# Performance work log

Hardware: AMD Instinct MI355X
Metric: run time of the kernel (lower is better)

## Reference

```python
import jax, jax.numpy as jnp
import numpy as np

LATENT_SIZE = 1024
WORD_SIZE = 64
NB_WORD = 8192
COMMIT_VQ = 2.5
BATCH = 2048


def setup_inputs() -> dict:
    key = jax.random.key(0)
    k1, k2, k3 = jax.random.split(key, 3)
    z_mean = jax.random.normal(k1, (BATCH, LATENT_SIZE), dtype=jnp.float32)
    z_log_var = jax.random.normal(k2, (BATCH, LATENT_SIZE), dtype=jnp.float32)
    # Embedding initialized uniform(-1/nb_word, 1/nb_word) in the torch module;
    # use normal here for a numerically non-degenerate correctness baseline.
    emb_weight = jax.random.normal(k3, (NB_WORD, WORD_SIZE), dtype=jnp.float32)
    return {"z_mean": z_mean, "z_log_var": z_log_var, "emb_weight": emb_weight}


def reference(z_mean, z_log_var, emb_weight):
    sg = jax.lax.stop_gradient
    input_shape = z_mean.shape
    # (B * latent/word, word)
    z = z_mean.reshape(-1, LATENT_SIZE // WORD_SIZE, WORD_SIZE)
    z_flat = z.reshape(-1, WORD_SIZE)
    # squared euclidean distances: (N, nb_word)
    distances = (
        jnp.sum(z_flat ** 2, axis=1, keepdims=True)
        + jnp.sum(emb_weight ** 2, axis=1)
        - 2.0 * jnp.einsum("bd,nd->bn", z_flat, emb_weight)
    )
    min_idx = jnp.argmin(distances, axis=1)  # (N,)
    z_q = emb_weight[min_idx].reshape(z.shape)  # gather codebook vectors
    loss = (
        jnp.mean((sg(z_q) - z) ** 2)
        + COMMIT_VQ * jnp.mean((z_q - sg(z)) ** 2)
    )
    z_q_st = z + sg(z_q - z)  # straight-through estimator
    return z_q_st.reshape(input_shape), loss
```

## Files before the change

kernel.cpp:

```cpp
#include <hip/hip_runtime.h>
#include <math.h>

#define LATENT   1024
#define WORD     64
#define NB_WORD  8192
#define BATCH    2048
#define NROWS    (BATCH * LATENT / WORD)
#define NELEM    (BATCH * LATENT)

#define NCHUNK   8
#define CWCHUNK  (NB_WORD / NCHUNK)
#define TPC      (CWCHUNK / 16)
#define NTILE    (NB_WORD / 16)
#define PKTS     (NTILE * 6 * 64)

typedef __attribute__((ext_vector_type(8))) __bf16 bf16x8;
typedef __attribute__((ext_vector_type(4))) float  f32x4;

__global__ __launch_bounds__(256) void vq_prep_kernel(
    const float* __restrict__ emb, float* __restrict__ e2,
    bf16x8* __restrict__ epack) {
    int m = blockIdx.x * 256 + threadIdx.x;
    int tile = m >> 4, l15 = m & 15;
    float s0 = 0.f, s1 = 0.f, s2 = 0.f, s3 = 0.f;
#pragma unroll
    for (int Ks = 0; Ks < 2; ++Ks) {
#pragma unroll
        for (int q = 0; q < 4; ++q) {
            const float4* s4 = reinterpret_cast<const float4*>(
                emb + (size_t)m * WORD + Ks * 32 + q * 8);
            float4 a = s4[0], b = s4[1];
            float tv[8] = {a.x, a.y, a.z, a.w, b.x, b.y, b.z, b.w};
            bf16x8 oh, om, ol;
#pragma unroll
            for (int e = 0; e < 8; ++e) {
                float v = tv[e];
                if ((e & 3) == 0) s0 = fmaf(v, v, s0);
                else if ((e & 3) == 1) s1 = fmaf(v, v, s1);
                else if ((e & 3) == 2) s2 = fmaf(v, v, s2);
                else s3 = fmaf(v, v, s3);
                __bf16 h  = (__bf16)v;
                float r1  = v - (float)h;
                __bf16 mm = (__bf16)r1;
                float r2  = r1 - (float)mm;
                __bf16 lo = (__bf16)r2;
                oh[e] = h; om[e] = mm; ol[e] = lo;
            }
            size_t base = ((size_t)tile * 6) * 64 + q * 16 + l15;
            epack[base + (size_t)(0 * 2 + Ks) * 64] = oh;
            epack[base + (size_t)(1 * 2 + Ks) * 64] = om;
            epack[base + (size_t)(2 * 2 + Ks) * 64] = ol;
        }
    }
    e2[m] = (s0 + s1) + (s2 + s3);
}

__device__ __forceinline__ void gload_lds16(const char* g, char* l) {
    __builtin_amdgcn_global_load_lds(
        (const __attribute__((address_space(1))) void*)g,
        (__attribute__((address_space(3))) void*)l, 16, 0, 0);
}

#define MFMA16 __builtin_amdgcn_mfma_f32_16x16x32_bf16

__global__ __launch_bounds__(256)
__attribute__((amdgpu_waves_per_eu(4, 4)))
void vq_argmin_kernel(
    const float* __restrict__ z, const bf16x8* __restrict__ epack,
    const float* __restrict__ e2, unsigned long long* __restrict__ best) {

    __shared__ __align__(16) char le[4][2][6144];

    const int tid   = threadIdx.x;
    const int lane  = tid & 63;
    const int wband = tid >> 6;
    const int l15   = lane & 15;
    const int l4    = lane >> 4;
    const int rowbase   = blockIdx.x * 128 + wband * 32;
    const int tile0     = blockIdx.y * TPC;
    const int chunkbase = blockIdx.y * CWCHUNK;
    const float* e2g    = e2 + chunkbase;
    const int off       = (blockIdx.x & 15) * 4;

    bf16x8 A[2][2][3];
    const float4* zf4 = reinterpret_cast<const float4*>(z);
#pragma unroll
    for (int mt = 0; mt < 2; ++mt) {
        int row = rowbase + mt * 16 + l15;
#pragma unroll
        for (int Ks = 0; Ks < 2; ++Ks) {
            float4 v0 = zf4[(size_t)row * 16 + Ks * 8 + l4 * 2];
            float4 v1 = zf4[(size_t)row * 16 + Ks * 8 + l4 * 2 + 1];
            float tv[8] = {v0.x, v0.y, v0.z, v0.w, v1.x, v1.y, v1.z, v1.w};
#pragma unroll
            for (int e = 0; e < 8; ++e) {
                float v = tv[e];
                __bf16 h  = (__bf16)v;
                float r1  = v - (float)h;
                __bf16 m  = (__bf16)r1;
                float r2  = r1 - (float)m;
                __bf16 lo = (__bf16)r2;
                A[mt][Ks][0][e] = h;
                A[mt][Ks][1][e] = m;
                A[mt][Ks][2][e] = lo;
            }
        }
    }

    char* lbase = &le[wband][0][0];

    {
        const char* src = (const char*)epack + (size_t)(tile0 + off) * 6144 + lane * 16;
#pragma unroll
        for (int j = 0; j < 6; ++j)
            gload_lds16(src + j * 1024, lbase + j * 1024);
    }
    float e2A = e2g[off * 16 + l15];
    float e2B;

    float bestd[8] = {INFINITY, INFINITY, INFINITY, INFINITY,
                      INFINITY, INFINITY, INFINITY, INFINITY};
    int   bt[8]    = {0, 0, 0, 0, 0, 0, 0, 0};

#define PHASE(BUFOFF, E2CUR, E2NXT, TCUR, TNXT)                             \
    {                                                                       \
        const char* srcn = (const char*)epack +                             \
                           (size_t)(tile0 + (TNXT)) * 6144 + lane * 16;     \
        char* dstn = lbase + ((BUFOFF) ^ 6144);                             \
        _Pragma("unroll")                                                   \
        for (int j = 0; j < 6; ++j)                                         \
            gload_lds16(srcn + j * 1024, dstn + j * 1024);                  \
        E2NXT = e2g[(TNXT) * 16 + l15];                                     \
        asm volatile("s_waitcnt vmcnt(7)" ::: "memory");                    \
        asm volatile("" :: "v"(E2CUR));         \
        const char* bb = lbase + (BUFOFF) + lane * 16;                      \
        bf16x8 Bh0 = *reinterpret_cast<const bf16x8*>(bb);                  \
        bf16x8 Bh1 = *reinterpret_cast<const bf16x8*>(bb + 1024);           \
        bf16x8 Bm0 = *reinterpret_cast<const bf16x8*>(bb + 2048);           \
        bf16x8 Bm1 = *reinterpret_cast<const bf16x8*>(bb + 3072);           \
        bf16x8 Bl0 = *reinterpret_cast<const bf16x8*>(bb + 4096);           \
        bf16x8 Bl1 = *reinterpret_cast<const bf16x8*>(bb + 5120);           \
        f32x4 a00 = {0.f, 0.f, 0.f, 0.f};                                   \
        f32x4 a01 = {0.f, 0.f, 0.f, 0.f};                                   \
        f32x4 a10 = {0.f, 0.f, 0.f, 0.f};                                   \
        f32x4 a11 = {0.f, 0.f, 0.f, 0.f};                                   \
          \
        a00 = MFMA16(A[0][0][0], Bh0, a00, 0, 0, 0);                        \
        a10 = MFMA16(A[1][0][0], Bh0, a10, 0, 0, 0);                        \
        a01 = MFMA16(A[0][1][0], Bh1, a01, 0, 0, 0);                        \
        a11 = MFMA16(A[1][1][0], Bh1, a11, 0, 0, 0);                        \
        a00 = MFMA16(A[0][0][1], Bh0, a00, 0, 0, 0);                        \
        a10 = MFMA16(A[1][0][1], Bh0, a10, 0, 0, 0);                        \
        a01 = MFMA16(A[0][1][1], Bh1, a01, 0, 0, 0);                        \
        a11 = MFMA16(A[1][1][1], Bh1, a11, 0, 0, 0);                        \
        a00 = MFMA16(A[0][0][2], Bh0, a00, 0, 0, 0);                        \
        a10 = MFMA16(A[1][0][2], Bh0, a10, 0, 0, 0);                        \
        a01 = MFMA16(A[0][1][2], Bh1, a01, 0, 0, 0);                        \
        a11 = MFMA16(A[1][1][2], Bh1, a11, 0, 0, 0);                        \
        a00 = MFMA16(A[0][0][1], Bm0, a00, 0, 0, 0);                        \
        a10 = MFMA16(A[1][0][1], Bm0, a10, 0, 0, 0);                        \
        a01 = MFMA16(A[0][1][1], Bm1, a01, 0, 0, 0);                        \
        a11 = MFMA16(A[1][1][1], Bm1, a11, 0, 0, 0);                        \
        a00 = MFMA16(A[0][0][0], Bm0, a00, 0, 0, 0);                        \
        a10 = MFMA16(A[1][0][0], Bm0, a10, 0, 0, 0);                        \
        a01 = MFMA16(A[0][1][0], Bm1, a01, 0, 0, 0);                        \
        a11 = MFMA16(A[1][1][0], Bm1, a11, 0, 0, 0);                        \
        a00 = MFMA16(A[0][0][0], Bl0, a00, 0, 0, 0);                        \
        a10 = MFMA16(A[1][0][0], Bl0, a10, 0, 0, 0);                        \
        a01 = MFMA16(A[0][1][0], Bl1, a01, 0, 0, 0);                        \
        a11 = MFMA16(A[1][1][0], Bl1, a11, 0, 0, 0);                        \
        _Pragma("unroll")                                                   \
        for (int v = 0; v < 4; ++v) {                                       \
            float d0 = fmaf(-2.0f, a00[v] + a01[v], E2CUR);                 \
            if (d0 < bestd[v])     { bestd[v]     = d0; bt[v]     = (TCUR); } \
            float d1 = fmaf(-2.0f, a10[v] + a11[v], E2CUR);                 \
            if (d1 < bestd[4 + v]) { bestd[4 + v] = d1; bt[4 + v] = (TCUR); } \
        }                                                                   \
    }

    int t0 = off;
    for (int tt = 0; tt < TPC; tt += 2) {
        int t1 = t0 + 1; if (t1 >= TPC) t1 -= TPC;
        int t2 = t1 + 1; if (t2 >= TPC) t2 -= TPC;
        PHASE(0,    e2A, e2B, t0, t1);
        PHASE(6144, e2B, e2A, t1, t2);
        t0 = t2;
    }
#undef PHASE

#pragma unroll
    for (int mt = 0; mt < 2; ++mt) {
#pragma unroll
        for (int v = 0; v < 4; ++v) {
            float bd = bestd[mt * 4 + v];
            int   cw = chunkbase + bt[mt * 4 + v] * 16 + l15;
            unsigned db = __float_as_uint(bd);
            db = (db & 0x80000000u) ? ~db : (db | 0x80000000u);
            unsigned long long key =
                ((unsigned long long)db << 32) | (unsigned)cw;
#pragma unroll
            for (int off2 = 1; off2 < 16; off2 <<= 1) {
                unsigned long long o = __shfl_xor(key, off2);
                key = (o < key) ? o : key;
            }
            if (l15 == 0)
                atomicMin(&best[rowbase + mt * 16 + l4 * 4 + v], key);
        }
    }
}

__global__ __launch_bounds__(256) void vq_out_kernel(
    const float* __restrict__ z, const float* __restrict__ emb,
    const unsigned long long* __restrict__ best,
    float* __restrict__ out, float* __restrict__ lsum) {
    const int base = (blockIdx.x * 256 + threadIdx.x) * 8;
    const int row  = base >> 6;
    const int m    = (int)(best[row] & 0xFFFFFFFFull);

    const float4* zp = reinterpret_cast<const float4*>(z + base);
    const float4* qp = reinterpret_cast<const float4*>(emb + (size_t)m * WORD + (base & 63));
    float4* op = reinterpret_cast<float4*>(out + base);

    float s = 0.f;
#pragma unroll
    for (int i = 0; i < 2; ++i) {
        float4 zv = zp[i];
        float4 qv = qp[i];
        float dx = qv.x - zv.x, dy = qv.y - zv.y, dz = qv.z - zv.z, dw = qv.w - zv.w;
        float4 ov;
        ov.x = zv.x + dx; ov.y = zv.y + dy; ov.z = zv.z + dz; ov.w = zv.w + dw;
        op[i] = ov;
        s += dx*dx + dy*dy + dz*dz + dw*dw;
    }

#pragma unroll
    for (int off = 32; off > 0; off >>= 1) s += __shfl_down(s, off);
    __shared__ float wsum[4];
    int lane = threadIdx.x & 63, wid = threadIdx.x >> 6;
    if (lane == 0) wsum[wid] = s;
    __syncthreads();
    if (threadIdx.x == 0)
        atomicAdd(lsum, (wsum[0] + wsum[1]) + (wsum[2] + wsum[3]));
}

__global__ void vq_loss_kernel(const float* __restrict__ lsum,
                               float* __restrict__ loss_out) {
    float mean = lsum[0] * (1.0f / (float)NELEM);
    loss_out[0] = mean + 2.5f * mean;
}

extern "C" void kernel_launch(void* const* d_in, const int* in_sizes, int n_in,
                              void* d_out, int out_size, void* d_ws, size_t ws_size,
                              hipStream_t stream) {
    const float* z   = (const float*)d_in[0];
    const float* emb = (const float*)d_in[2];
    float* out = (float*)d_out;

    bf16x8* epack = (bf16x8*)d_ws;
    float*  e2    = (float*)((char*)d_ws + (size_t)PKTS * 16);
    unsigned long long* best =
        (unsigned long long*)((char*)e2 + NB_WORD * sizeof(float));
    float* lsum = (float*)((char*)best + NROWS * sizeof(unsigned long long));

    hipMemsetAsync(best, 0xFF, NROWS * sizeof(unsigned long long), stream);
    hipMemsetAsync(lsum, 0, sizeof(float), stream);

    vq_prep_kernel<<<NB_WORD / 256, 256, 0, stream>>>(emb, e2, epack);
    vq_argmin_kernel<<<dim3(NROWS / 128, NCHUNK), 256, 0, stream>>>(
        z, epack, e2, best);
    vq_out_kernel<<<NELEM / (256 * 8), 256, 0, stream>>>(z, emb, best, out, lsum);
    vq_loss_kernel<<<1, 1, 0, stream>>>(lsum, out + NELEM);
}
```

Baseline: 222.3 us.

## Share codebook LDS tiles across waves and overlap argmin fold with MFMAs

The four waves of a block now cooperatively load one shared double-buffered codebook tile into LDS and synchronise with a block barrier, instead of each wave streaming its own private copy. The argmin fold for the previous tile is software-pipelined and interleaved between MFMA groups of the current tile using sched_barrier and setprio. Occupancy is pinned to 3 waves per EU, and blocks get staggered start delays via s_sleep. This cuts redundant global-to-LDS traffic and hides the fold latency, at the cost of a per-tile block barrier and lower occupancy.

```diff
diff --git a/kernel.cpp b/kernel.cpp
--- a/kernel.cpp
+++ b/kernel.cpp
@@ -62,14 +62,22 @@
 }
 
 #define MFMA16 __builtin_amdgcn_mfma_f32_16x16x32_bf16
+#define SBAR() __builtin_amdgcn_sched_barrier(0)
 
 __global__ __launch_bounds__(256)
-__attribute__((amdgpu_waves_per_eu(4, 4)))
+__attribute__((amdgpu_waves_per_eu(3, 3)))
 void vq_argmin_kernel(
     const float* __restrict__ z, const bf16x8* __restrict__ epack,
     const float* __restrict__ e2, unsigned long long* __restrict__ best) {
 
-    __shared__ __align__(16) char le[4][2][6144];
+    {
+        int ph = blockIdx.x & 3;
+        if (ph == 1) __builtin_amdgcn_s_sleep(2);
+        else if (ph == 2) __builtin_amdgcn_s_sleep(4);
+        else if (ph == 3) __builtin_amdgcn_s_sleep(6);
+    }
+
+    __shared__ __align__(16) char le[2 * 6144];
 
     const int tid   = threadIdx.x;
     const int lane  = tid & 63;
@@ -107,86 +115,101 @@
         }
     }
 
-    char* lbase = &le[wband][0][0];
-
     {
-        const char* src = (const char*)epack + (size_t)(tile0 + off) * 6144 + lane * 16;
-#pragma unroll
-        for (int j = 0; j < 6; ++j)
-            gload_lds16(src + j * 1024, lbase + j * 1024);
-    }
-    float e2A = e2g[off * 16 + l15];
-    float e2B;
+        const char* src = (const char*)epack + (size_t)(tile0 + off) * 6144;
+        gload_lds16(src + wband * 1024 + lane * 16, le + wband * 1024);
+        if (wband < 2)
+            gload_lds16(src + (4 + wband) * 1024 + lane * 16,
+                        le + (4 + wband) * 1024);
+    }
 
     float bestd[8] = {INFINITY, INFINITY, INFINITY, INFINITY,
                       INFINITY, INFINITY, INFINITY, INFINITY};
     int   bt[8]    = {0, 0, 0, 0, 0, 0, 0, 0};
 
-#define PHASE(BUFOFF, E2CUR, E2NXT, TCUR, TNXT)                             \
+    f32x4 x00, x01, x10, x11;
+    f32x4 y00 = {0.f,0.f,0.f,0.f}, y01 = {0.f,0.f,0.f,0.f};
+    f32x4 y10 = {0.f,0.f,0.f,0.f}, y11 = {0.f,0.f,0.f,0.f};
+    float e2x, e2y = INFINITY;
+
+#define FOLD1(P00,P01,P10,P11, E2P, TP, V)                                  \
+    do {                                                                    \
+        float d0_ = fmaf(-2.0f, P00[V] + P01[V], E2P);                      \
+        if (d0_ < bestd[V])     { bestd[V]     = d0_; bt[V]     = (TP); }   \
+        float d1_ = fmaf(-2.0f, P10[V] + P11[V], E2P);                      \
+        if (d1_ < bestd[4+(V)]) { bestd[4+(V)] = d1_; bt[4+(V)] = (TP); }   \
+    } while (0)
+
+#define GROUP(SPL, B0, B1, C00,C01,C10,C11)                                 \
+    C00 = MFMA16(A[0][0][SPL], B0, C00, 0, 0, 0);                           \
+    C10 = MFMA16(A[1][0][SPL], B0, C10, 0, 0, 0);                           \
+    C01 = MFMA16(A[0][1][SPL], B1, C01, 0, 0, 0);                           \
+    C11 = MFMA16(A[1][1][SPL], B1, C11, 0, 0, 0);
+
+#define PHASE(BUFOFF, C00,C01,C10,C11, P00,P01,P10,P11, E2C, E2P, TCUR, TNXT, TP) \
     {                                                                       \
-        const char* srcn = (const char*)epack +                             \
-                           (size_t)(tile0 + (TNXT)) * 6144 + lane * 16;     \
-        char* dstn = lbase + ((BUFOFF) ^ 6144);                             \
-        _Pragma("unroll")                                                   \
-        for (int j = 0; j < 6; ++j)                                         \
-            gload_lds16(srcn + j * 1024, dstn + j * 1024);                  \
-        E2NXT = e2g[(TNXT) * 16 + l15];                                     \
-        asm volatile("s_waitcnt vmcnt(7)" ::: "memory");                    \
-        asm volatile("" :: "v"(E2CUR));         \
-        const char* bb = lbase + (BUFOFF) + lane * 16;                      \
+        asm volatile("s_waitcnt vmcnt(0)" ::: "memory");                    \
+        SBAR();                                                             \
+        __builtin_amdgcn_s_barrier();          \
+        const char* bb = le + (BUFOFF) + lane * 16;                         \
         bf16x8 Bh0 = *reinterpret_cast<const bf16x8*>(bb);                  \
         bf16x8 Bh1 = *reinterpret_cast<const bf16x8*>(bb + 1024);           \
         bf16x8 Bm0 = *reinterpret_cast<const bf16x8*>(bb + 2048);           \
         bf16x8 Bm1 = *reinterpret_cast<const bf16x8*>(bb + 3072);           \
         bf16x8 Bl0 = *reinterpret_cast<const bf16x8*>(bb + 4096);           \
         bf16x8 Bl1 = *reinterpret_cast<const bf16x8*>(bb + 5120);           \
-        f32x4 a00 = {0.f, 0.f, 0.f, 0.f};                                   \
-        f32x4 a01 = {0.f, 0.f, 0.f, 0.f};                                   \
-        f32x4 a10 = {0.f, 0.f, 0.f, 0.f};                                   \
-        f32x4 a11 = {0.f, 0.f, 0.f, 0.f};                                   \
-          \
-        a00 = MFMA16(A[0][0][0], Bh0, a00, 0, 0, 0);                        \
-        a10 = MFMA16(A[1][0][0], Bh0, a10, 0, 0, 0);                        \
-        a01 = MFMA16(A[0][1][0], Bh1, a01, 0, 0, 0);                        \
-        a11 = MFMA16(A[1][1][0], Bh1, a11, 0, 0, 0);                        \
-        a00 = MFMA16(A[0][0][1], Bh0, a00, 0, 0, 0);                        \
-        a10 = MFMA16(A[1][0][1], Bh0, a10, 0, 0, 0);                        \
-        a01 = MFMA16(A[0][1][1], Bh1, a01, 0, 0, 0);                        \
-        a11 = MFMA16(A[1][1][1], Bh1, a11, 0, 0, 0);                        \
-        a00 = MFMA16(A[0][0][2], Bh0, a00, 0, 0, 0);                        \
-        a10 = MFMA16(A[1][0][2], Bh0, a10, 0, 0, 0);                        \
-        a01 = MFMA16(A[0][1][2], Bh1, a01, 0, 0, 0);                        \
-        a11 = MFMA16(A[1][1][2], Bh1, a11, 0, 0, 0);                        \
-        a00 = MFMA16(A[0][0][1], Bm0, a00, 0, 0, 0);                        \
-        a10 = MFMA16(A[1][0][1], Bm0, a10, 0, 0, 0);                        \
-        a01 = MFMA16(A[0][1][1], Bm1, a01, 0, 0, 0);                        \
-        a11 = MFMA16(A[1][1][1], Bm1, a11, 0, 0, 0);                        \
-        a00 = MFMA16(A[0][0][0], Bm0, a00, 0, 0, 0);                        \
-        a10 = MFMA16(A[1][0][0], Bm0, a10, 0, 0, 0);                        \
-        a01 = MFMA16(A[0][1][0], Bm1, a01, 0, 0, 0);                        \
-        a11 = MFMA16(A[1][1][0], Bm1, a11, 0, 0, 0);                        \
-        a00 = MFMA16(A[0][0][0], Bl0, a00, 0, 0, 0);                        \
-        a10 = MFMA16(A[1][0][0], Bl0, a10, 0, 0, 0);                        \
-        a01 = MFMA16(A[0][1][0], Bl1, a01, 0, 0, 0);                        \
-        a11 = MFMA16(A[1][1][0], Bl1, a11, 0, 0, 0);                        \
-        _Pragma("unroll")                                                   \
-        for (int v = 0; v < 4; ++v) {                                       \
-            float d0 = fmaf(-2.0f, a00[v] + a01[v], E2CUR);                 \
-            if (d0 < bestd[v])     { bestd[v]     = d0; bt[v]     = (TCUR); } \
-            float d1 = fmaf(-2.0f, a10[v] + a11[v], E2CUR);                 \
-            if (d1 < bestd[4 + v]) { bestd[4 + v] = d1; bt[4 + v] = (TCUR); } \
-        }                                                                   \
+        const char* srcn = (const char*)epack +                             \
+                           (size_t)(tile0 + (TNXT)) * 6144;                 \
+        char* dstn = le + ((BUFOFF) ^ 6144);                                \
+        gload_lds16(srcn + wband * 1024 + lane * 16, dstn + wband * 1024);  \
+        if (wband < 2)                                                      \
+            gload_lds16(srcn + (4 + wband) * 1024 + lane * 16,              \
+                        dstn + (4 + wband) * 1024);                         \
+        E2C = e2g[(TCUR) * 16 + l15];                                       \
+        __builtin_amdgcn_s_setprio(1);                                      \
+        SBAR();                                                             \
+                \
+        FOLD1(P00,P01,P10,P11, E2P, TP, 0);                                 \
+        FOLD1(P00,P01,P10,P11, E2P, TP, 1);                                 \
+        C00 = (f32x4){0.f,0.f,0.f,0.f};                                     \
+        C01 = (f32x4){0.f,0.f,0.f,0.f};                                     \
+        C10 = (f32x4){0.f,0.f,0.f,0.f};                                     \
+        C11 = (f32x4){0.f,0.f,0.f,0.f};                                     \
+        SBAR();                                                             \
+        GROUP(0, Bh0, Bh1, C00,C01,C10,C11)                         \
+        SBAR();                                                             \
+        FOLD1(P00,P01,P10,P11, E2P, TP, 2);                                 \
+        SBAR();                                                             \
+        GROUP(1, Bh0, Bh1, C00,C01,C10,C11)                         \
+        SBAR();                                                             \
+        FOLD1(P00,P01,P10,P11, E2P, TP, 3);                                 \
+        SBAR();                                                             \
+        GROUP(2, Bh0, Bh1, C00,C01,C10,C11)                         \
+        GROUP(1, Bm0, Bm1, C00,C01,C10,C11)                         \
+        GROUP(0, Bm0, Bm1, C00,C01,C10,C11)                         \
+        GROUP(0, Bl0, Bl1, C00,C01,C10,C11)                         \
+        __builtin_amdgcn_s_setprio(0);                                      \
     }
 
     int t0 = off;
+    int tp = 0;
     for (int tt = 0; tt < TPC; tt += 2) {
         int t1 = t0 + 1; if (t1 >= TPC) t1 -= TPC;
         int t2 = t1 + 1; if (t2 >= TPC) t2 -= TPC;
-        PHASE(0,    e2A, e2B, t0, t1);
-        PHASE(6144, e2B, e2A, t1, t2);
+        PHASE(0,    x00,x01,x10,x11, y00,y01,y10,y11, e2x, e2y, t0, t1, tp);
+        PHASE(6144, y00,y01,y10,y11, x00,x01,x10,x11, e2y, e2x, t1, t2, t0);
+        tp = t1;
         t0 = t2;
     }
 #undef PHASE
+
+    asm volatile("s_waitcnt vmcnt(0)" ::: "memory");
+    FOLD1(y00,y01,y10,y11, e2y, tp, 0);
+    FOLD1(y00,y01,y10,y11, e2y, tp, 1);
+    FOLD1(y00,y01,y10,y11, e2y, tp, 2);
+    FOLD1(y00,y01,y10,y11, e2y, tp, 3);
+#undef FOLD1
+#undef GROUP
 
 #pragma unroll
     for (int mt = 0; mt < 2; ++mt) {
```

New measurement: 200.1 us. 1.11x faster.

## Switch argmin to 32x32x16 MFMA with block-shared codebook tiles

Applied to the files above, without the earlier changes.

Replaces the 16x16x32 bf16 MFMA tiling with 32x32x16 tiles that cover 32 rows by 32 codewords per wave, so one accumulator holds the whole K=64 reduction. The codebook pack layout is changed to match, and the four waves now share one double-buffered LDS tile loaded cooperatively under a block barrier, instead of each wave keeping private buffers. It also staggers block start with s_sleep, raises MFMA priority with setprio, and lowers the occupancy target to 3 waves per EU. The aim is fewer B-operand loads and a better MFMA-to-overhead ratio, at the cost of a full vmcnt(0) wait plus barrier on every phase and wider 32-lane shuffle reductions.

```diff
diff --git a/kernel.cpp b/kernel.cpp
--- a/kernel.cpp
+++ b/kernel.cpp
@@ -10,47 +10,43 @@
 
 #define NCHUNK   8
 #define CWCHUNK  (NB_WORD / NCHUNK)
-#define TPC      (CWCHUNK / 16)
-#define NTILE    (NB_WORD / 16)
-#define PKTS     (NTILE * 6 * 64)
-
-typedef __attribute__((ext_vector_type(8))) __bf16 bf16x8;
-typedef __attribute__((ext_vector_type(4))) float  f32x4;
+#define TPC      32
+#define PKTS     (NB_WORD / 32 * 768)
+
+typedef __attribute__((ext_vector_type(8)))  __bf16 bf16x8;
+typedef __attribute__((ext_vector_type(16))) float  f32x16;
 
 __global__ __launch_bounds__(256) void vq_prep_kernel(
     const float* __restrict__ emb, float* __restrict__ e2,
     bf16x8* __restrict__ epack) {
     int m = blockIdx.x * 256 + threadIdx.x;
-    int tile = m >> 4, l15 = m & 15;
+    int tile = m >> 5, col = m & 31;
     float s0 = 0.f, s1 = 0.f, s2 = 0.f, s3 = 0.f;
 #pragma unroll
-    for (int Ks = 0; Ks < 2; ++Ks) {
-#pragma unroll
-        for (int q = 0; q < 4; ++q) {
-            const float4* s4 = reinterpret_cast<const float4*>(
-                emb + (size_t)m * WORD + Ks * 32 + q * 8);
-            float4 a = s4[0], b = s4[1];
-            float tv[8] = {a.x, a.y, a.z, a.w, b.x, b.y, b.z, b.w};
-            bf16x8 oh, om, ol;
-#pragma unroll
-            for (int e = 0; e < 8; ++e) {
-                float v = tv[e];
-                if ((e & 3) == 0) s0 = fmaf(v, v, s0);
-                else if ((e & 3) == 1) s1 = fmaf(v, v, s1);
-                else if ((e & 3) == 2) s2 = fmaf(v, v, s2);
-                else s3 = fmaf(v, v, s3);
-                __bf16 h  = (__bf16)v;
-                float r1  = v - (float)h;
-                __bf16 mm = (__bf16)r1;
-                float r2  = r1 - (float)mm;
-                __bf16 lo = (__bf16)r2;
-                oh[e] = h; om[e] = mm; ol[e] = lo;
-            }
-            size_t base = ((size_t)tile * 6) * 64 + q * 16 + l15;
-            epack[base + (size_t)(0 * 2 + Ks) * 64] = oh;
-            epack[base + (size_t)(1 * 2 + Ks) * 64] = om;
-            epack[base + (size_t)(2 * 2 + Ks) * 64] = ol;
+    for (int g = 0; g < 8; ++g) {
+        const float4* s4 = reinterpret_cast<const float4*>(
+            emb + (size_t)m * WORD + g * 8);
+        float4 a = s4[0], b = s4[1];
+        float tv[8] = {a.x, a.y, a.z, a.w, b.x, b.y, b.z, b.w};
+        bf16x8 oh, om, ol;
+#pragma unroll
+        for (int e = 0; e < 8; ++e) {
+            float v = tv[e];
+            if ((e & 3) == 0) s0 = fmaf(v, v, s0);
+            else if ((e & 3) == 1) s1 = fmaf(v, v, s1);
+            else if ((e & 3) == 2) s2 = fmaf(v, v, s2);
+            else s3 = fmaf(v, v, s3);
+            __bf16 h  = (__bf16)v;
+            float r1  = v - (float)h;
+            __bf16 mm = (__bf16)r1;
+            float r2  = r1 - (float)mm;
+            oh[e] = h; om[e] = mm; ol[e] = (__bf16)r2;
         }
+        int ks = g >> 1, hi = g & 1;
+        size_t pb = (size_t)tile * 768;
+        epack[pb + (size_t)(0 * 4 + ks) * 64 + hi * 32 + col] = oh;
+        epack[pb + (size_t)(1 * 4 + ks) * 64 + hi * 32 + col] = om;
+        epack[pb + (size_t)(2 * 4 + ks) * 64 + hi * 32 + col] = ol;
     }
     e2[m] = (s0 + s1) + (s2 + s3);
 }
@@ -61,36 +57,42 @@
         (__attribute__((address_space(3))) void*)l, 16, 0, 0);
 }
 
-#define MFMA16 __builtin_amdgcn_mfma_f32_16x16x32_bf16
+#define MFMA32 __builtin_amdgcn_mfma_f32_32x32x16_bf16
 
 __global__ __launch_bounds__(256)
-__attribute__((amdgpu_waves_per_eu(4, 4)))
+__attribute__((amdgpu_waves_per_eu(3, 3)))
 void vq_argmin_kernel(
     const float* __restrict__ z, const bf16x8* __restrict__ epack,
     const float* __restrict__ e2, unsigned long long* __restrict__ best) {
 
-    __shared__ __align__(16) char le[4][2][6144];
+    {
+        int ph = blockIdx.x & 3;
+        if (ph == 1) __builtin_amdgcn_s_sleep(2);
+        else if (ph == 2) __builtin_amdgcn_s_sleep(4);
+        else if (ph == 3) __builtin_amdgcn_s_sleep(6);
+    }
+
+    __shared__ __align__(16) char le[2 * 12288];
 
     const int tid   = threadIdx.x;
     const int lane  = tid & 63;
     const int wband = tid >> 6;
-    const int l15   = lane & 15;
-    const int l4    = lane >> 4;
+    const int l31   = lane & 31;
+    const int hi    = lane >> 5;
     const int rowbase   = blockIdx.x * 128 + wband * 32;
     const int tile0     = blockIdx.y * TPC;
     const int chunkbase = blockIdx.y * CWCHUNK;
     const float* e2g    = e2 + chunkbase;
-    const int off       = (blockIdx.x & 15) * 4;
-
-    bf16x8 A[2][2][3];
-    const float4* zf4 = reinterpret_cast<const float4*>(z);
-#pragma unroll
-    for (int mt = 0; mt < 2; ++mt) {
-        int row = rowbase + mt * 16 + l15;
-#pragma unroll
-        for (int Ks = 0; Ks < 2; ++Ks) {
-            float4 v0 = zf4[(size_t)row * 16 + Ks * 8 + l4 * 2];
-            float4 v1 = zf4[(size_t)row * 16 + Ks * 8 + l4 * 2 + 1];
+    const int off       = (blockIdx.x & 7) * 4;
+
+    bf16x8 A[4][3];
+    {
+        const float4* zf4 = reinterpret_cast<const float4*>(
+            z + (size_t)(rowbase + l31) * WORD);
+#pragma unroll
+        for (int ks = 0; ks < 4; ++ks) {
+            float4 v0 = zf4[ks * 4 + hi * 2];
+            float4 v1 = zf4[ks * 4 + hi * 2 + 1];
             float tv[8] = {v0.x, v0.y, v0.z, v0.w, v1.x, v1.y, v1.z, v1.w};
 #pragma unroll
             for (int e = 0; e < 8; ++e) {
@@ -99,113 +101,114 @@
                 float r1  = v - (float)h;
                 __bf16 m  = (__bf16)r1;
                 float r2  = r1 - (float)m;
-                __bf16 lo = (__bf16)r2;
-                A[mt][Ks][0][e] = h;
-                A[mt][Ks][1][e] = m;
-                A[mt][Ks][2][e] = lo;
+                A[ks][0][e] = h;
+                A[ks][1][e] = m;
+                A[ks][2][e] = (__bf16)r2;
             }
         }
     }
 
-    char* lbase = &le[wband][0][0];
-
     {
-        const char* src = (const char*)epack + (size_t)(tile0 + off) * 6144 + lane * 16;
-#pragma unroll
-        for (int j = 0; j < 6; ++j)
-            gload_lds16(src + j * 1024, lbase + j * 1024);
-    }
-    float e2A = e2g[off * 16 + l15];
+        const char* src = (const char*)epack + (size_t)(tile0 + off) * 12288 + tid * 16;
+        char* dst = le + (tid & ~63) * 16;
+        gload_lds16(src,        dst);
+        gload_lds16(src + 4096, dst + 4096);
+        gload_lds16(src + 8192, dst + 8192);
+    }
+    float e2A = e2g[off * 32 + l31];
     float e2B;
 
-    float bestd[8] = {INFINITY, INFINITY, INFINITY, INFINITY,
-                      INFINITY, INFINITY, INFINITY, INFINITY};
-    int   bt[8]    = {0, 0, 0, 0, 0, 0, 0, 0};
-
-#define PHASE(BUFOFF, E2CUR, E2NXT, TCUR, TNXT)                             \
+    float bestd[16];
+    int   bt[16];
+#pragma unroll
+    for (int v = 0; v < 16; ++v) { bestd[v] = INFINITY; bt[v] = 0; }
+
+#define PHASE(BUFOFF, E2C, E2N, TCUR, TNXT)                                 \
     {                                                                       \
+        asm volatile("s_waitcnt vmcnt(0)" ::: "memory");                    \
+        __builtin_amdgcn_sched_barrier(0);                                  \
+        __builtin_amdgcn_s_barrier();          \
         const char* srcn = (const char*)epack +                             \
-                           (size_t)(tile0 + (TNXT)) * 6144 + lane * 16;     \
-        char* dstn = lbase + ((BUFOFF) ^ 6144);                             \
-        _Pragma("unroll")                                                   \
-        for (int j = 0; j < 6; ++j)                                         \
-            gload_lds16(srcn + j * 1024, dstn + j * 1024);                  \
-        E2NXT = e2g[(TNXT) * 16 + l15];                                     \
-        asm volatile("s_waitcnt vmcnt(7)" ::: "memory");                    \
-        asm volatile("" :: "v"(E2CUR));         \
-        const char* bb = lbase + (BUFOFF) + lane * 16;                      \
+                           (size_t)(tile0 + (TNXT)) * 12288 + tid * 16;     \
+        char* dstn = le + ((BUFOFF) ^ 12288) + (tid & ~63) * 16;            \
+        gload_lds16(srcn,        dstn);                                     \
+        gload_lds16(srcn + 4096, dstn + 4096);                              \
+        gload_lds16(srcn + 8192, dstn + 8192);                              \
+        E2N = e2g[(TNXT) * 32 + l31];                                       \
+        const char* bb = le + (BUFOFF) + lane * 16;                         \
         bf16x8 Bh0 = *reinterpret_cast<const bf16x8*>(bb);                  \
         bf16x8 Bh1 = *reinterpret_cast<const bf16x8*>(bb + 1024);           \
-        bf16x8 Bm0 = *reinterpret_cast<const bf16x8*>(bb + 2048);           \
-        bf16x8 Bm1 = *reinterpret_cast<const bf16x8*>(bb + 3072);           \
-        bf16x8 Bl0 = *reinterpret_cast<const bf16x8*>(bb + 4096);           \
-        bf16x8 Bl1 = *reinterpret_cast<const bf16x8*>(bb + 5120);           \
-        f32x4 a00 = {0.f, 0.f, 0.f, 0.f};                                   \
-        f32x4 a01 = {0.f, 0.f, 0.f, 0.f};                                   \
-        f32x4 a10 = {0.f, 0.f, 0.f, 0.f};                                   \
-        f32x4 a11 = {0.f, 0.f, 0.f, 0.f};                                   \
-          \
-        a00 = MFMA16(A[0][0][0], Bh0, a00, 0, 0, 0);                        \
-        a10 = MFMA16(A[1][0][0], Bh0, a10, 0, 0, 0);                        \
-        a01 = MFMA16(A[0][1][0], Bh1, a01, 0, 0, 0);                        \
-        a11 = MFMA16(A[1][1][0], Bh1, a11, 0, 0, 0);                        \
-        a00 = MFMA16(A[0][0][1], Bh0, a00, 0, 0, 0);                        \
-        a10 = MFMA16(A[1][0][1], Bh0, a10, 0, 0, 0);                        \
-        a01 = MFMA16(A[0][1][1], Bh1, a01, 0, 0, 0);                        \
-        a11 = MFMA16(A[1][1][1], Bh1, a11, 0, 0, 0);                        \
-        a00 = MFMA16(A[0][0][2], Bh0, a00, 0, 0, 0);                        \
-        a10 = MFMA16(A[1][0][2], Bh0, a10, 0, 0, 0);                        \
-        a01 = MFMA16(A[0][1][2], Bh1, a01, 0, 0, 0);                        \
-        a11 = MFMA16(A[1][1][2], Bh1, a11, 0, 0, 0);                        \
-        a00 = MFMA16(A[0][0][1], Bm0, a00, 0, 0, 0);                        \
-        a10 = MFMA16(A[1][0][1], Bm0, a10, 0, 0, 0);                        \
-        a01 = MFMA16(A[0][1][1], Bm1, a01, 0, 0, 0);                        \
-        a11 = MFMA16(A[1][1][1], Bm1, a11, 0, 0, 0);                        \
-        a00 = MFMA16(A[0][0][0], Bm0, a00, 0, 0, 0);                        \
-        a10 = MFMA16(A[1][0][0], Bm0, a10, 0, 0, 0);                        \
-        a01 = MFMA16(A[0][1][0], Bm1, a01, 0, 0, 0);                        \
-        a11 = MFMA16(A[1][1][0], Bm1, a11, 0, 0, 0);                        \
-        a00 = MFMA16(A[0][0][0], Bl0, a00, 0, 0, 0);                        \
-        a10 = MFMA16(A[1][0][0], Bl0, a10, 0, 0, 0);                        \
-        a01 = MFMA16(A[0][1][0], Bl1, a01, 0, 0, 0);                        \
-        a11 = MFMA16(A[1][1][0], Bl1, a11, 0, 0, 0);                        \
+        bf16x8 Bh2 = *reinterpret_cast<const bf16x8*>(bb + 2048);           \
+        bf16x8 Bh3 = *reinterpret_cast<const bf16x8*>(bb + 3072);           \
+        bf16x8 Bm0 = *reinterpret_cast<const bf16x8*>(bb + 4096);           \
+        bf16x8 Bm1 = *reinterpret_cast<const bf16x8*>(bb + 5120);           \
+        bf16x8 Bm2 = *reinterpret_cast<const bf16x8*>(bb + 6144);           \
+        bf16x8 Bm3 = *reinterpret_cast<const bf16x8*>(bb + 7168);           \
+        bf16x8 Bl0 = *reinterpret_cast<const bf16x8*>(bb + 8192);           \
+        bf16x8 Bl1 = *reinterpret_cast<const bf16x8*>(bb + 9216);           \
+        bf16x8 Bl2 = *reinterpret_cast<const bf16x8*>(bb + 10240);          \
+        bf16x8 Bl3 = *reinterpret_cast<const bf16x8*>(bb + 11264);          \
+        f32x16 acc = {0.f,0.f,0.f,0.f,0.f,0.f,0.f,0.f,                      \
+                      0.f,0.f,0.f,0.f,0.f,0.f,0.f,0.f};                     \
+        __builtin_amdgcn_s_setprio(1);                                      \
+                                        \
+        acc = MFMA32(A[0][0], Bh0, acc, 0, 0, 0);                           \
+        acc = MFMA32(A[0][1], Bh0, acc, 0, 0, 0);                           \
+        acc = MFMA32(A[0][2], Bh0, acc, 0, 0, 0);                           \
+        acc = MFMA32(A[0][1], Bm0, acc, 0, 0, 0);                           \
+        acc = MFMA32(A[0][0], Bm0, acc, 0, 0, 0);                           \
+        acc = MFMA32(A[0][0], Bl0, acc, 0, 0, 0);                           \
+        acc = MFMA32(A[1][0], Bh1, acc, 0, 0, 0);                           \
+        acc = MFMA32(A[1][1], Bh1, acc, 0, 0, 0);                           \
+        acc = MFMA32(A[1][2], Bh1, acc, 0, 0, 0);                           \
+        acc = MFMA32(A[1][1], Bm1, acc, 0, 0, 0);                           \
+        acc = MFMA32(A[1][0], Bm1, acc, 0, 0, 0);                           \
+        acc = MFMA32(A[1][0], Bl1, acc, 0, 0, 0);                           \
+        acc = MFMA32(A[2][0], Bh2, acc, 0, 0, 0);                           \
+        acc = MFMA32(A[2][1], Bh2, acc, 0, 0, 0);                           \
+        acc = MFMA32(A[2][2], Bh2, acc, 0, 0, 0);                           \
+        acc = MFMA32(A[2][1], Bm2, acc, 0, 0, 0);                           \
+        acc = MFMA32(A[2][0], Bm2, acc, 0, 0, 0);                           \
+        acc = MFMA32(A[2][0], Bl2, acc, 0, 0, 0);                           \
+        acc = MFMA32(A[3][0], Bh3, acc, 0, 0, 0);                           \
+        acc = MFMA32(A[3][1], Bh3, acc, 0, 0, 0);                           \
+        acc = MFMA32(A[3][2], Bh3, acc, 0, 0, 0);                           \
+        acc = MFMA32(A[3][1], Bm3, acc, 0, 0, 0);                           \
+        acc = MFMA32(A[3][0], Bm3, acc, 0, 0, 0);                           \
+        acc = MFMA32(A[3][0], Bl3, acc, 0, 0, 0);                           \
+        __builtin_amdgcn_s_setprio(0);                                      \
         _Pragma("unroll")                                                   \
-        for (int v = 0; v < 4; ++v) {                                       \
-            float d0 = fmaf(-2.0f, a00[v] + a01[v], E2CUR);                 \
-            if (d0 < bestd[v])     { bestd[v]     = d0; bt[v]     = (TCUR); } \
-            float d1 = fmaf(-2.0f, a10[v] + a11[v], E2CUR);                 \
-            if (d1 < bestd[4 + v]) { bestd[4 + v] = d1; bt[4 + v] = (TCUR); } \
+        for (int v = 0; v < 16; ++v) {                                      \
+            float d = fmaf(-2.0f, acc[v], E2C);                             \
+            if (d < bestd[v]) { bestd[v] = d; bt[v] = (TCUR); }             \
         }                                                                   \
     }
 
     int t0 = off;
     for (int tt = 0; tt < TPC; tt += 2) {
-        int t1 = t0 + 1; if (t1 >= TPC) t1 -= TPC;
-        int t2 = t1 + 1; if (t2 >= TPC) t2 -= TPC;
-        PHASE(0,    e2A, e2B, t0, t1);
-        PHASE(6144, e2B, e2A, t1, t2);
+        int t1 = (t0 + 1) & (TPC - 1);
+        int t2 = (t0 + 2) & (TPC - 1);
+        PHASE(0,     e2A, e2B, t0, t1);
+        PHASE(12288, e2B, e2A, t1, t2);
         t0 = t2;
     }
 #undef PHASE
 
 #pragma unroll
-    for (int mt = 0; mt < 2; ++mt) {
-#pragma unroll
-        for (int v = 0; v < 4; ++v) {
-            float bd = bestd[mt * 4 + v];
-            int   cw = chunkbase + bt[mt * 4 + v] * 16 + l15;
-            unsigned db = __float_as_uint(bd);
-            db = (db & 0x80000000u) ? ~db : (db | 0x80000000u);
-            unsigned long long key =
-                ((unsigned long long)db << 32) | (unsigned)cw;
-#pragma unroll
-            for (int off2 = 1; off2 < 16; off2 <<= 1) {
-                unsigned long long o = __shfl_xor(key, off2);
-                key = (o < key) ? o : key;
-            }
-            if (l15 == 0)
-                atomicMin(&best[rowbase + mt * 16 + l4 * 4 + v], key);
+    for (int v = 0; v < 16; ++v) {
+        float bd = bestd[v];
+        int   cw = chunkbase + bt[v] * 32 + l31;
+        unsigned db = __float_as_uint(bd);
+        db = (db & 0x80000000u) ? ~db : (db | 0x80000000u);
+        unsigned long long key =
+            ((unsigned long long)db << 32) | (unsigned)cw;
+#pragma unroll
+        for (int o = 1; o < 32; o <<= 1) {
+            unsigned long long other = __shfl_xor(key, o);
+            key = (other < key) ? other : key;
         }
+        if (l31 == 0)
+            atomicMin(&best[rowbase + (v & 3) + 8 * (v >> 2) + 4 * hi], key);
     }
 }
 
```

Result: no change. 219.6 us (-1.2%).
